# Optimization experiments

Hardware: AMD Instinct MI355X
Metric: run time of the kernel (lower is better)

## Reference

```python
import jax, jax.numpy as jnp
import numpy as np

N_NODES = 50000
N_EDGES = 100000
NUM_GRAPHS = 1024
EMB = 600
NUM_ATOMIC = 119      # Num_atomic_number
NUM_HYB = 8           # HybridizationType values
NUM_AROM = 2
NUM_CHIR = 4          # ChiralType values
NUM_CHARGE = 9
NUM_BOND_TYPE = 22    # BondType values


def setup_inputs() -> dict:
    key = jax.random.key(0)
    ks = jax.random.split(key, 20)
    # integer graph data
    atom = jnp.stack([
        jax.random.randint(ks[0], (N_NODES,), 0, NUM_ATOMIC),
        jax.random.randint(ks[1], (N_NODES,), 0, NUM_HYB),
        jax.random.randint(ks[2], (N_NODES,), 0, NUM_AROM),
        jax.random.randint(ks[3], (N_NODES,), 0, NUM_CHIR),
        jax.random.randint(ks[4], (N_NODES,), 0, NUM_CHARGE),
    ], axis=1)
    bond_index = jax.random.randint(ks[5], (2, N_EDGES), 0, N_NODES)
    bond_attr = jnp.stack([
        jax.random.randint(ks[6], (N_EDGES,), 0, NUM_BOND_TYPE),
        jax.random.randint(ks[7], (N_EDGES,), 0, NUM_ATOMIC),
    ], axis=1)
    batch = jnp.sort(jax.random.randint(ks[8], (N_NODES,), 0, NUM_GRAPHS))
    # parameters (kaiming-uniform-ish scale)
    def emb(k, n, d):
        bound = float(np.sqrt(6.0 / d))
        return jax.random.uniform(k, (n, d), minval=-bound, maxval=bound, dtype=jnp.float32)
    def lin(k, out_d, in_d):
        bound = float(np.sqrt(6.0 / in_d))
        return jax.random.uniform(k, (out_d, in_d), minval=-bound, maxval=bound, dtype=jnp.float32)
    return {
        "atom": atom, "bond_index": bond_index, "bond_attr": bond_attr, "batch": batch,
        "W_atom_num": emb(ks[9], NUM_ATOMIC, EMB),
        "W_hyb": emb(ks[10], NUM_HYB, EMB),
        "W_arom": emb(ks[11], NUM_AROM, EMB),
        "W_chir": emb(ks[12], NUM_CHIR, EMB),
        "W_charge": emb(ks[13], NUM_CHARGE, EMB),
        "W_bond_type": emb(ks[14], NUM_BOND_TYPE, EMB),
        "W_bond_atom_i": emb(ks[15], NUM_ATOMIC, EMB),
        "W_sl_atom": emb(ks[16], NUM_ATOMIC, EMB),
        "W_sl": emb(ks[17], 1, EMB),
        "W1": lin(ks[18], EMB, EMB), "b1": jnp.zeros((EMB,), jnp.float32),
        "W2": lin(ks[19], EMB // 2, EMB), "b2": jnp.zeros((EMB // 2,), jnp.float32),
        "W3": lin(jax.random.fold_in(key, 99), 1, EMB // 2),
    }


def reference(atom, bond_index, bond_attr, batch,
              W_atom_num, W_hyb, W_arom, W_chir, W_charge,
              W_bond_type, W_bond_atom_i, W_sl_atom, W_sl,
              W1, b1, W2, b2, W3):
    N = atom.shape[0]
    # Step 1: node embedding = sum of 5 lookups  [N, EMB]
    node = (W_atom_num[atom[:, 0]] + W_hyb[atom[:, 1]] + W_arom[atom[:, 2]]
            + W_chir[atom[:, 3]] + W_charge[atom[:, 4]])
    # Step 2: edge embeddings; self-loops appended after real bonds
    bond_emb = W_bond_type[bond_attr[:, 0]] + W_bond_atom_i[bond_attr[:, 1]]  # [E, EMB]
    sl_emb = W_sl_atom[atom[:, 0]] + W_sl[0]                                  # [N, EMB]
    edge_emb = jnp.concatenate([bond_emb, sl_emb], axis=0)                    # [E+N, EMB]
    loop = jnp.arange(N, dtype=bond_index.dtype)
    src = jnp.concatenate([bond_index[0], loop])
    dst = jnp.concatenate([bond_index[1], loop])
    # Step 3: 2 message-passing layers: gather src, multiply edge_emb, scatter-add to dst
    for _ in range(2):
        node = jax.ops.segment_sum(node[src] * edge_emb, dst, num_segments=N)
    # Step 4: energy MLP  ReLU -> Linear(d,d) -> ReLU -> Linear(d,d/2) -> ReLU -> Linear(d/2,1)
    h = jax.nn.relu(node)
    h = jax.nn.relu(h @ W1.T + b1)
    h = jax.nn.relu(h @ W2.T + b2)
    node_energy = h @ W3.T  # [N, 1]
    # Step 5: global add pool per graph
    dg = jax.ops.segment_sum(node_energy, batch, num_segments=NUM_GRAPHS)  # [NUM_GRAPHS, 1]
    return dg
```

## Files before the change

### kernel.cpp

```cpp
#include <hip/hip_runtime.h>

#define EMB 600
#define Q4  150
#define KP  608

typedef unsigned short ushortT;
typedef __attribute__((ext_vector_type(8))) short short8;
typedef __attribute__((ext_vector_type(4))) short short4v;
typedef __attribute__((ext_vector_type(4))) float f32x4;

__device__ __forceinline__ float4 f4add(float4 a, float4 b) {
    return make_float4(a.x + b.x, a.y + b.y, a.z + b.z, a.w + b.w);
}
__device__ __forceinline__ float4 f4fma(float4 acc, float4 v, float4 e) {
    return make_float4(fmaf(v.x, e.x, acc.x), fmaf(v.y, e.y, acc.y),
                       fmaf(v.z, e.z, acc.z), fmaf(v.w, e.w, acc.w));
}
__device__ __forceinline__ ushortT bf16_rne(float x) {
    unsigned u = __float_as_uint(x);
    return (ushortT)((u + 0x7fffu + ((u >> 16) & 1u)) >> 16);
}
__device__ __forceinline__ float bf16_to_f(ushortT h) {
    return __uint_as_float(((unsigned)h) << 16);
}

__device__ __forceinline__ size_t frag_off(int row, int col) {
    return ((size_t)((row >> 4) * 19 + (col >> 5)) * 64
            + (row & 15) + 16 * ((col >> 3) & 3)) * 8 + (col & 7);
}

__global__ void k_node_embed(const int* __restrict__ atom,
                             const float4* __restrict__ Wa,
                             const float4* __restrict__ Wh,
                             const float4* __restrict__ War,
                             const float4* __restrict__ Wc,
                             const float4* __restrict__ Wch,
                             float4* __restrict__ out, int N) {
    int idx = blockIdx.x * blockDim.x + threadIdx.x;
    int total = N * Q4;
    if (idx >= total) return;
    int n = idx / Q4;
    int q = idx - n * Q4;
    const int* a = atom + n * 5;
    float4 r = Wa[a[0] * Q4 + q];
    r = f4add(r, Wh [a[1] * Q4 + q]);
    r = f4add(r, War[a[2] * Q4 + q]);
    r = f4add(r, Wc [a[3] * Q4 + q]);
    r = f4add(r, Wch[a[4] * Q4 + q]);
    out[idx] = r;
}

__global__ void k_hist(const int* __restrict__ bdst, int* __restrict__ counts, int E) {
    int i = blockIdx.x * blockDim.x + threadIdx.x;
    if (i < E) atomicAdd(&counts[bdst[i]], 1);
}

__global__ __launch_bounds__(256) void k_scan_l1(const int* __restrict__ counts,
                                                 int* __restrict__ offsets,
                                                 int* __restrict__ blocksums, int N) {
    __shared__ int s[256];
    int t = threadIdx.x;
    int i = blockIdx.x * 256 + t;
    int v = (i < N) ? counts[i] : 0;
    s[t] = v;
    __syncthreads();
#pragma unroll
    for (int off = 1; off < 256; off <<= 1) {
        int x = (t >= off) ? s[t - off] : 0;
        __syncthreads();
        s[t] += x;
        __syncthreads();
    }
    if (i < N) offsets[i] = s[t] - v;
    if (t == 255) blocksums[blockIdx.x] = s[255];
}

__global__ __launch_bounds__(256) void k_scan_l2(int* __restrict__ blocksums,
                                                 int* __restrict__ blockpref, int nb) {
    __shared__ int s[256];
    int t = threadIdx.x;
    int v = (t < nb) ? blocksums[t] : 0;
    s[t] = v;
    __syncthreads();
#pragma unroll
    for (int off = 1; off < 256; off <<= 1) {
        int x = (t >= off) ? s[t - off] : 0;
        __syncthreads();
        s[t] += x;
        __syncthreads();
    }
    if (t < nb) blockpref[t] = s[t] - v;
}

__global__ __launch_bounds__(256) void k_scan_l3(int* __restrict__ offsets,
                                                 int* __restrict__ cursor,
                                                 const int* __restrict__ blockpref, int N) {
    int i = blockIdx.x * 256 + threadIdx.x;
    if (i < N) {
        int o = offsets[i] + blockpref[blockIdx.x];
        offsets[i] = o;
        cursor[i]  = o;
    }
}

__global__ void k_scatter(const int* __restrict__ bdst, int* __restrict__ cursor,
                          int* __restrict__ edge_list, int E) {
    int i = blockIdx.x * blockDim.x + threadIdx.x;
    if (i < E) {
        int pos = atomicAdd(&cursor[bdst[i]], 1);
        edge_list[pos] = i;
    }
}

__global__ __launch_bounds__(256) void k_mp_gather(
        const int* __restrict__ bsrc, const int* __restrict__ battr,
        const int* __restrict__ atom,
        const int* __restrict__ offsets, const int* __restrict__ counts,
        const int* __restrict__ edge_list,
        const float4* __restrict__ Wbt, const float4* __restrict__ Wbai,
        const float4* __restrict__ Wsla, const float4* __restrict__ Wsl,
        const float4* __restrict__ in, float4* __restrict__ out, int N) {
    int wid  = (int)((blockIdx.x * blockDim.x + threadIdx.x) >> 6);
    int lane = threadIdx.x & 63;
    int d    = wid >> 1;
    int half = wid & 1;
    if (d >= N) return;
    int q1 = 75 * half + lane;
    int q2 = q1 + 64;
    bool has2 = lane < 11;

    int start = offsets[d], cnt = counts[d];
    int s = 0, t0 = 0, t1 = 0;
    if (cnt > 0) {
        int eid = edge_list[start];
        s  = bsrc[eid];
        t0 = battr[eid * 2 + 0];
        t1 = battr[eid * 2 + 1];
    }

    const float4* slA = Wsla + atom[d * 5] * Q4;
    const float4* inr = in + (size_t)d * Q4;
    float4 acc1 = make_float4(0, 0, 0, 0), acc2 = acc1;
    acc1 = f4fma(acc1, inr[q1], f4add(slA[q1], Wsl[q1]));
    if (has2) acc2 = f4fma(acc2, inr[q2], f4add(slA[q2], Wsl[q2]));

    for (int k = 0; k < cnt; k++) {
        int ns = s, nt0 = t0, nt1 = t1;
        if (k + 1 < cnt) {
            int ne = edge_list[start + k + 1];
            ns  = bsrc[ne];
            nt0 = battr[ne * 2 + 0];
            nt1 = battr[ne * 2 + 1];
        }
        const float4* e0 = Wbt  + t0 * Q4;
        const float4* e1 = Wbai + t1 * Q4;
        const float4* sr = in + (size_t)s * Q4;
        acc1 = f4fma(acc1, sr[q1], f4add(e0[q1], e1[q1]));
        if (has2) acc2 = f4fma(acc2, sr[q2], f4add(e0[q2], e1[q2]));
        s = ns; t0 = nt0; t1 = nt1;
    }
    float4* orow = out + (size_t)d * Q4;
    orow[q1] = acc1;
    if (has2) orow[q2] = acc2;
}

__device__ __forceinline__ void frag_store4h(ushortT* __restrict__ hi,
                                             int d, int q, float4 v) {
    int kc = q >> 3, ks = (q >> 1) & 3, halfw = q & 1;
    size_t off = ((size_t)((d >> 4) * 19 + kc) * 64 + (d & 15) + 16 * ks) * 8
                 + halfw * 4;
    float vv[4] = {v.x, v.y, v.z, v.w};
    short4v h4;
#pragma unroll
    for (int j = 0; j < 4; j++)
        h4[j] = (short)bf16_rne(fmaxf(vv[j], 0.f));
    *(short4v*)(hi + off) = h4;
}

__global__ __launch_bounds__(256) void k_mp_gather_rs(
        const int* __restrict__ bsrc, const int* __restrict__ battr,
        const int* __restrict__ atom,
        const int* __restrict__ offsets, const int* __restrict__ counts,
        const int* __restrict__ edge_list,
        const float4* __restrict__ Wbt, const float4* __restrict__ Wbai,
        const float4* __restrict__ Wsla, const float4* __restrict__ Wsl,
        const float4* __restrict__ in,
        ushortT* __restrict__ hi, int N) {
    int wid  = (int)((blockIdx.x * blockDim.x + threadIdx.x) >> 6);
    int lane = threadIdx.x & 63;
    int d    = wid >> 1;
    int half = wid & 1;
    if (d >= N) return;
    int q1 = 75 * half + lane;
    int q2 = q1 + 64;
    bool has2 = lane < 11;

    int start = offsets[d], cnt = counts[d];
    int s = 0, t0 = 0, t1 = 0;
    if (cnt > 0) {
        int eid = edge_list[start];
        s  = bsrc[eid];
        t0 = battr[eid * 2 + 0];
        t1 = battr[eid * 2 + 1];
    }

    const float4* slA = Wsla + atom[d * 5] * Q4;
    const float4* inr = in + (size_t)d * Q4;
    float4 acc1 = make_float4(0, 0, 0, 0), acc2 = acc1;
    acc1 = f4fma(acc1, inr[q1], f4add(slA[q1], Wsl[q1]));
    if (has2) acc2 = f4fma(acc2, inr[q2], f4add(slA[q2], Wsl[q2]));

    for (int k = 0; k < cnt; k++) {
        int ns = s, nt0 = t0, nt1 = t1;
        if (k + 1 < cnt) {
            int ne = edge_list[start + k + 1];
            ns  = bsrc[ne];
            nt0 = battr[ne * 2 + 0];
            nt1 = battr[ne * 2 + 1];
        }
        const float4* e0 = Wbt  + t0 * Q4;
        const float4* e1 = Wbai + t1 * Q4;
        const float4* sr = in + (size_t)s * Q4;
        acc1 = f4fma(acc1, sr[q1], f4add(e0[q1], e1[q1]));
        if (has2) acc2 = f4fma(acc2, sr[q2], f4add(e0[q2], e1[q2]));
        s = ns; t0 = nt0; t1 = nt1;
    }
    frag_store4h(hi, d, q1, acc1);
    if (has2) frag_store4h(hi, d, q2, acc2);
    if (half == 0 && lane == 31) {
        size_t off = ((size_t)((d >> 4) * 19 + 18) * 64 + (d & 15) + 48) * 8;
        short8 z = {0, 0, 0, 0, 0, 0, 0, 0};
        *(short8*)(hi + off) = z;
    }
}

__global__ void k_split_w_frag(const float* __restrict__ src,
                               short8* __restrict__ dhi, short8* __restrict__ dlo,
                               int rows_in, int cb_count) {
    int idx = blockIdx.x * blockDim.x + threadIdx.x;
    int total = cb_count * 19 * 64;
    if (idx >= total) return;
    int lane = idx & 63;
    int tile = idx >> 6;
    int cb = tile / 19, kc = tile - cb * 19;
    int col = cb * 16 + (lane & 15);
    int k0  = kc * 32 + (lane >> 4) * 8;
    short8 h, l;
#pragma unroll
    for (int j = 0; j < 8; j++) {
        int k = k0 + j;
        float x = (col < rows_in && k < 600) ? src[(size_t)col * 600 + k] : 0.f;
        ushortT hh = bf16_rne(x);
        h[j] = (short)hh;
        l[j] = (short)bf16_rne(x - bf16_to_f(hh));
    }
    dhi[idx] = h;
    dlo[idx] = l;
}

struct FragSet { short8 a[4], bh[4], bl[4]; };

__device__ __forceinline__ void frag_load(FragSet& f,
        const short8* __restrict__ Af,
        const short8* __restrict__ Bfh, const short8* __restrict__ Bfl,
        int aBase, int bBase, int kc) {
    int ak = aBase + kc * 64;
    int bk = bBase + kc * 64;
#pragma unroll
    for (int i = 0; i < 4; i++) {
        f.a[i]  = Af [ak + i * 1216];
        f.bh[i] = Bfh[bk + i * 1216];
        f.bl[i] = Bfl[bk + i * 1216];
    }
}

__device__ __forceinline__ void frag_mfma(const FragSet& f, f32x4 acc[4][4]) {
#pragma unroll
    for (int i = 0; i < 4; i++)
#pragma unroll
        for (int j = 0; j < 4; j++) {
            acc[i][j] = __builtin_amdgcn_mfma_f32_16x16x32_bf16(f.a[i], f.bh[j], acc[i][j], 0, 0, 0);
            acc[i][j] = __builtin_amdgcn_mfma_f32_16x16x32_bf16(f.a[i], f.bl[j], acc[i][j], 0, 0, 0);
        }
}

__device__ __forceinline__ void gemm_core_reg(
        const short8* __restrict__ Af,
        const short8* __restrict__ Bfh, const short8* __restrict__ Bfl,
        int aBase, int bBase, f32x4 acc[4][4]) {
    for (int kc = 0; kc < 19; kc++) {
        FragSet f;
        frag_load(f, Af, Bfh, Bfl, aBase, bBase, kc);
        frag_mfma(f, acc);
    }
}

__device__ __forceinline__ void decode_wg(int ncb, int& rowblk, int& colblk) {
    int nwg  = gridDim.x;
    int orig = blockIdx.x;
    int q = nwg >> 3, r = nwg & 7;
    int xcd = orig & 7, rank = orig >> 3;
    int wgid = (xcd < r ? xcd * (q + 1) : r * (q + 1) + (xcd - r) * q) + rank;
    rowblk = wgid / ncb;
    colblk = wgid - rowblk * ncb;
}

__global__ __launch_bounds__(256, 4) void k_gemm1r(
        const short8* __restrict__ Af,
        const short8* __restrict__ Wfh, const short8* __restrict__ Wfl,
        const float* __restrict__ b1,
        ushortT* __restrict__ Hf, int N) {
    int rowblk, colblk;
    decode_wg(5, rowblk, colblk);
    int row0 = rowblk * 128;
    int col0 = colblk * 128;
    int t = threadIdx.x, w = t >> 6, l = t & 63;
    int wr = w >> 1, wc = w & 1, fr = l & 15, fq = l >> 4;

    int aBase = (rowblk * 8 + wr * 4) * 1216 + l;
    int bBase = (colblk * 8 + wc * 4) * 1216 + l;
    f32x4 acc[4][4];
#pragma unroll
    for (int i = 0; i < 4; i++)
#pragma unroll
        for (int j = 0; j < 4; j++) acc[i][j] = f32x4{0.f, 0.f, 0.f, 0.f};
    gemm_core_reg(Af, Wfh, Wfl, aBase, bBase, acc);

#pragma unroll
    for (int i = 0; i < 4; i++) {
#pragma unroll
        for (int j = 0; j < 4; j++) {
            int col = col0 + wc * 64 + j * 16 + fr;
            float bias = (col < 600) ? b1[col] : 0.f;
#pragma unroll
            for (int r = 0; r < 4; r++) {
                int row = row0 + wr * 64 + i * 16 + fq * 4 + r;
                if (row >= N) continue;
                if (col < 600) {
                    float x = fmaxf(acc[i][j][r] + bias, 0.f);
                    Hf[frag_off(row, col)] = bf16_rne(x);
                } else if (col < KP) {
                    Hf[frag_off(row, col)] = 0;
                }
            }
        }
    }
}

__global__ __launch_bounds__(256, 4) void k_gemm2r(
        const short8* __restrict__ Af,
        const short8* __restrict__ Wfh, const short8* __restrict__ Wfl,
        const float* __restrict__ b2, const float* __restrict__ W3,
        float* __restrict__ energy, int N) {
    __shared__ float sE[128];
    int rowblk, colblk;
    decode_wg(3, rowblk, colblk);
    int row0 = rowblk * 128;
    int col0 = colblk * 128;
    int t = threadIdx.x, w = t >> 6, l = t & 63;
    int wr = w >> 1, wc = w & 1, fr = l & 15, fq = l >> 4;

    int aBase = (rowblk * 8 + wr * 4) * 1216 + l;
    int bBase = (colblk * 8 + wc * 4) * 1216 + l;
    f32x4 acc[4][4];
#pragma unroll
    for (int i = 0; i < 4; i++)
#pragma unroll
        for (int j = 0; j < 4; j++) acc[i][j] = f32x4{0.f, 0.f, 0.f, 0.f};
    gemm_core_reg(Af, Wfh, Wfl, aBase, bBase, acc);

    if (t < 128) sE[t] = 0.f;
    __syncthreads();
#pragma unroll
    for (int i = 0; i < 4; i++) {
        float p[4] = {0.f, 0.f, 0.f, 0.f};
#pragma unroll
        for (int j = 0; j < 4; j++) {
            int col = col0 + wc * 64 + j * 16 + fr;
            if (col < 300) {
                float bias = b2[col];
                float wv   = W3[col];
#pragma unroll
                for (int r = 0; r < 4; r++)
                    p[r] += fmaxf(acc[i][j][r] + bias, 0.f) * wv;
            }
        }
#pragma unroll
        for (int r = 0; r < 4; r++) {
            float v = p[r];
            v += __shfl_xor(v, 1, 64);
            v += __shfl_xor(v, 2, 64);
            v += __shfl_xor(v, 4, 64);
            v += __shfl_xor(v, 8, 64);
            p[r] = v;
        }
        if (fr == 0) {
#pragma unroll
            for (int r = 0; r < 4; r++)
                atomicAdd(&sE[wr * 64 + i * 16 + fq * 4 + r], p[r]);
        }
    }
    __syncthreads();
    if (t < 128) {
        int row = row0 + t;
        if (row < N) atomicAdd(&energy[row], sE[t]);
    }
}

__global__ void k_pool(const float* __restrict__ energy, const int* __restrict__ batch,
                       float* __restrict__ dg, int N) {
    int i = blockIdx.x * blockDim.x + threadIdx.x;
    int lane = threadIdx.x & 63;
    float v = (i < N) ? energy[i] : 0.f;
    int   b = (i < N) ? batch[i]  : -1;
#pragma unroll
    for (int off = 1; off < 64; off <<= 1) {
        float vv = __shfl_down(v, off, 64);
        int   bb = __shfl_down(b, off, 64);
        if (lane + off < 64 && bb == b) v += vv;
    }
    int pb = __shfl_up(b, 1, 64);
    if (i < N && (lane == 0 || pb != b)) atomicAdd(&dg[b], v);
}

extern "C" void kernel_launch(void* const* d_in, const int* in_sizes, int n_in,
                              void* d_out, int out_size, void* d_ws, size_t ws_size,
                              hipStream_t stream) {
    const int* atom       = (const int*)d_in[0];
    const int* bond_index = (const int*)d_in[1];
    const int* bond_attr  = (const int*)d_in[2];
    const int* batch      = (const int*)d_in[3];
    const float* Wa   = (const float*)d_in[4];
    const float* Wh   = (const float*)d_in[5];
    const float* War  = (const float*)d_in[6];
    const float* Wc   = (const float*)d_in[7];
    const float* Wch  = (const float*)d_in[8];
    const float* Wbt  = (const float*)d_in[9];
    const float* Wbai = (const float*)d_in[10];
    const float* Wsla = (const float*)d_in[11];
    const float* Wsl  = (const float*)d_in[12];
    const float* W1   = (const float*)d_in[13];
    const float* b1   = (const float*)d_in[14];
    const float* W2   = (const float*)d_in[15];
    const float* b2   = (const float*)d_in[16];
    const float* W3   = (const float*)d_in[17];

    int N = in_sizes[0] / 5;
    int E = in_sizes[1] / 2;
    int Mb = (N + 127) / 128;
    int Npad = Mb * 128;
    int nTiles = Npad / 16;
    int nb = (N + 255) / 256;

    size_t regionBytes = (size_t)Npad * KP * 4;
    char* base = (char*)d_ws;
    float* nodeA = (float*)base;
    float* nodeB = (float*)(base + regionBytes);
    short8* Af = (short8*)nodeA;
    short8* Hf = (short8*)nodeB;
    char* tail = base + 2 * regionBytes;
    float* energy  = (float*)tail;
    int* counts    = (int*)(energy + N);
    int* offsets   = counts + N;
    int* cursor    = offsets + N;
    int* edge_list = cursor + N;
    short8* W1fh   = (short8*)(edge_list + E);
    short8* W1fl   = W1fh + 40 * 19 * 64;
    short8* W2fh   = W1fl + 40 * 19 * 64;
    short8* W2fl   = W2fh + 24 * 19 * 64;
    int* blocksums = (int*)(W2fl + 24 * 19 * 64);
    int* blockpref = blocksums + 256;

    const int* bsrc = bond_index;
    const int* bdst = bond_index + E;

    hipMemsetAsync(counts, 0, (size_t)N * sizeof(int), stream);
    k_hist<<<(E + 255) / 256, 256, 0, stream>>>(bdst, counts, E);
    k_scan_l1<<<nb, 256, 0, stream>>>(counts, offsets, blocksums, N);
    k_scan_l2<<<1, 256, 0, stream>>>(blocksums, blockpref, nb);
    k_scan_l3<<<nb, 256, 0, stream>>>(offsets, cursor, blockpref, N);
    k_scatter<<<(E + 255) / 256, 256, 0, stream>>>(bdst, cursor, edge_list, E);

    k_split_w_frag<<<(40 * 19 * 64 + 255) / 256, 256, 0, stream>>>(W1, W1fh, W1fl, 600, 40);
    k_split_w_frag<<<(24 * 19 * 64 + 255) / 256, 256, 0, stream>>>(W2, W2fh, W2fl, 300, 24);

    {
        int total = N * Q4;
        k_node_embed<<<(total + 255) / 256, 256, 0, stream>>>(
            atom, (const float4*)Wa, (const float4*)Wh, (const float4*)War,
            (const float4*)Wc, (const float4*)Wch, (float4*)nodeA, N);
    }

    int mpblocks = (2 * N * 64 + 255) / 256;
    k_mp_gather<<<mpblocks, 256, 0, stream>>>(bsrc, bond_attr, atom,
        offsets, counts, edge_list,
        (const float4*)Wbt, (const float4*)Wbai, (const float4*)Wsla, (const float4*)Wsl,
        (const float4*)nodeA, (float4*)nodeB, N);

    {
        int firstPad = N / 16;
        size_t offB  = (size_t)firstPad * 1216 * 16;
        size_t cntB  = (size_t)(nTiles - firstPad) * 1216 * 16;
        if (cntB) hipMemsetAsync((char*)Af + offB, 0, cntB, stream);
    }

    k_mp_gather_rs<<<mpblocks, 256, 0, stream>>>(bsrc, bond_attr, atom,
        offsets, counts, edge_list,
        (const float4*)Wbt, (const float4*)Wbai, (const float4*)Wsla, (const float4*)Wsl,
        (const float4*)nodeB, (ushortT*)Af, N);

    k_gemm1r<<<Mb * 5, 256, 0, stream>>>(Af, W1fh, W1fl, b1, (ushortT*)Hf, N);

    hipMemsetAsync(energy, 0, (size_t)N * sizeof(float), stream);
    k_gemm2r<<<Mb * 3, 256, 0, stream>>>(Hf, W2fh, W2fl, b2, W3, energy, N);

    hipMemsetAsync(d_out, 0, (size_t)out_size * sizeof(float), stream);
    k_pool<<<(N + 255) / 256, 256, 0, stream>>>(energy, batch, (float*)d_out, N);
}
```

Before: 392.4 us.

## Store layer-1 node features in bf16 and drop lo-split weight MFMAs

The first message-passing layer now writes its output as bf16 instead of fp32, and the second layer gathers bf16 rows and converts them to float, halving the intermediate traffic. The MLP GEMMs drop the hi/lo bf16 split of the weights and use a single bf16 weight copy, halving the MFMA count and the weight-fragment loads. In exchange, precision falls in both the intermediate node features and the weights, which may affect tolerance against the fp32 reference.

After: 348.9 us. -11.1%, faster.

```diff
diff --git a/kernel.cpp b/kernel.cpp
--- a/kernel.cpp
+++ b/kernel.cpp
@@ -22,6 +22,18 @@
 }
 __device__ __forceinline__ float bf16_to_f(ushortT h) {
     return __uint_as_float(((unsigned)h) << 16);
+}
+__device__ __forceinline__ short4v f4_to_bf4(float4 v) {
+    short4v r;
+    r[0] = (short)bf16_rne(v.x);
+    r[1] = (short)bf16_rne(v.y);
+    r[2] = (short)bf16_rne(v.z);
+    r[3] = (short)bf16_rne(v.w);
+    return r;
+}
+__device__ __forceinline__ float4 bf4_to_f4(short4v h) {
+    return make_float4(bf16_to_f((ushortT)h[0]), bf16_to_f((ushortT)h[1]),
+                       bf16_to_f((ushortT)h[2]), bf16_to_f((ushortT)h[3]));
 }
 
 __device__ __forceinline__ size_t frag_off(int row, int col) {
@@ -112,14 +124,14 @@
     }
 }
 
-__global__ __launch_bounds__(256) void k_mp_gather(
+__global__ __launch_bounds__(256) void k_mp_gather_b(
         const int* __restrict__ bsrc, const int* __restrict__ battr,
         const int* __restrict__ atom,
         const int* __restrict__ offsets, const int* __restrict__ counts,
         const int* __restrict__ edge_list,
         const float4* __restrict__ Wbt, const float4* __restrict__ Wbai,
         const float4* __restrict__ Wsla, const float4* __restrict__ Wsl,
-        const float4* __restrict__ in, float4* __restrict__ out, int N) {
+        const float4* __restrict__ in, ushortT* __restrict__ out, int N) {
     int wid  = (int)((blockIdx.x * blockDim.x + threadIdx.x) >> 6);
     int lane = threadIdx.x & 63;
     int d    = wid >> 1;
@@ -159,9 +171,9 @@
         if (has2) acc2 = f4fma(acc2, sr[q2], f4add(e0[q2], e1[q2]));
         s = ns; t0 = nt0; t1 = nt1;
     }
-    float4* orow = out + (size_t)d * Q4;
-    orow[q1] = acc1;
-    if (has2) orow[q2] = acc2;
+    ushortT* orow = out + (size_t)d * EMB;
+    *(short4v*)(orow + q1 * 4) = f4_to_bf4(acc1);
+    if (has2) *(short4v*)(orow + q2 * 4) = f4_to_bf4(acc2);
 }
 
 __device__ __forceinline__ void frag_store4h(ushortT* __restrict__ hi,
@@ -184,7 +196,7 @@
         const int* __restrict__ edge_list,
         const float4* __restrict__ Wbt, const float4* __restrict__ Wbai,
         const float4* __restrict__ Wsla, const float4* __restrict__ Wsl,
-        const float4* __restrict__ in,
+        const ushortT* __restrict__ in,
         ushortT* __restrict__ hi, int N) {
     int wid  = (int)((blockIdx.x * blockDim.x + threadIdx.x) >> 6);
     int lane = threadIdx.x & 63;
@@ -205,10 +217,12 @@
     }
 
     const float4* slA = Wsla + atom[d * 5] * Q4;
-    const float4* inr = in + (size_t)d * Q4;
+    const ushortT* inr = in + (size_t)d * EMB;
     float4 acc1 = make_float4(0, 0, 0, 0), acc2 = acc1;
-    acc1 = f4fma(acc1, inr[q1], f4add(slA[q1], Wsl[q1]));
-    if (has2) acc2 = f4fma(acc2, inr[q2], f4add(slA[q2], Wsl[q2]));
+    acc1 = f4fma(acc1, bf4_to_f4(*(const short4v*)(inr + q1 * 4)),
+                 f4add(slA[q1], Wsl[q1]));
+    if (has2) acc2 = f4fma(acc2, bf4_to_f4(*(const short4v*)(inr + q2 * 4)),
+                           f4add(slA[q2], Wsl[q2]));
 
     for (int k = 0; k < cnt; k++) {
         int ns = s, nt0 = t0, nt1 = t1;
@@ -220,9 +234,11 @@
         }
         const float4* e0 = Wbt  + t0 * Q4;
         const float4* e1 = Wbai + t1 * Q4;
-        const float4* sr = in + (size_t)s * Q4;
-        acc1 = f4fma(acc1, sr[q1], f4add(e0[q1], e1[q1]));
-        if (has2) acc2 = f4fma(acc2, sr[q2], f4add(e0[q2], e1[q2]));
+        const ushortT* sr = in + (size_t)s * EMB;
+        acc1 = f4fma(acc1, bf4_to_f4(*(const short4v*)(sr + q1 * 4)),
+                     f4add(e0[q1], e1[q1]));
+        if (has2) acc2 = f4fma(acc2, bf4_to_f4(*(const short4v*)(sr + q2 * 4)),
+                               f4add(e0[q2], e1[q2]));
         s = ns; t0 = nt0; t1 = nt1;
     }
     frag_store4h(hi, d, q1, acc1);
@@ -235,7 +251,7 @@
 }
 
 __global__ void k_split_w_frag(const float* __restrict__ src,
-                               short8* __restrict__ dhi, short8* __restrict__ dlo,
+                               short8* __restrict__ dst,
                                int rows_in, int cb_count) {
     int idx = blockIdx.x * blockDim.x + threadIdx.x;
     int total = cb_count * 19 * 64;
@@ -245,32 +261,27 @@
     int cb = tile / 19, kc = tile - cb * 19;
     int col = cb * 16 + (lane & 15);
     int k0  = kc * 32 + (lane >> 4) * 8;
-    short8 h, l;
+    short8 h;
 #pragma unroll
     for (int j = 0; j < 8; j++) {
         int k = k0 + j;
         float x = (col < rows_in && k < 600) ? src[(size_t)col * 600 + k] : 0.f;
-        ushortT hh = bf16_rne(x);
-        h[j] = (short)hh;
-        l[j] = (short)bf16_rne(x - bf16_to_f(hh));
-    }
-    dhi[idx] = h;
-    dlo[idx] = l;
-}
-
-struct FragSet { short8 a[4], bh[4], bl[4]; };
+        h[j] = (short)bf16_rne(x);
+    }
+    dst[idx] = h;
+}
+
+struct FragSet { short8 a[4], b[4]; };
 
 __device__ __forceinline__ void frag_load(FragSet& f,
-        const short8* __restrict__ Af,
-        const short8* __restrict__ Bfh, const short8* __restrict__ Bfl,
+        const short8* __restrict__ Af, const short8* __restrict__ Bf,
         int aBase, int bBase, int kc) {
     int ak = aBase + kc * 64;
     int bk = bBase + kc * 64;
 #pragma unroll
     for (int i = 0; i < 4; i++) {
-        f.a[i]  = Af [ak + i * 1216];
-        f.bh[i] = Bfh[bk + i * 1216];
-        f.bl[i] = Bfl[bk + i * 1216];
+        f.a[i] = Af[ak + i * 1216];
+        f.b[i] = Bf[bk + i * 1216];
     }
 }
 
@@ -278,19 +289,16 @@
 #pragma unroll
     for (int i = 0; i < 4; i++)
 #pragma unroll
-        for (int j = 0; j < 4; j++) {
-            acc[i][j] = __builtin_amdgcn_mfma_f32_16x16x32_bf16(f.a[i], f.bh[j], acc[i][j], 0, 0, 0);
-            acc[i][j] = __builtin_amdgcn_mfma_f32_16x16x32_bf16(f.a[i], f.bl[j], acc[i][j], 0, 0, 0);
-        }
+        for (int j = 0; j < 4; j++)
+            acc[i][j] = __builtin_amdgcn_mfma_f32_16x16x32_bf16(f.a[i], f.b[j], acc[i][j], 0, 0, 0);
 }
 
 __device__ __forceinline__ void gemm_core_reg(
-        const short8* __restrict__ Af,
-        const short8* __restrict__ Bfh, const short8* __restrict__ Bfl,
+        const short8* __restrict__ Af, const short8* __restrict__ Bf,
         int aBase, int bBase, f32x4 acc[4][4]) {
     for (int kc = 0; kc < 19; kc++) {
         FragSet f;
-        frag_load(f, Af, Bfh, Bfl, aBase, bBase, kc);
+        frag_load(f, Af, Bf, aBase, bBase, kc);
         frag_mfma(f, acc);
     }
 }
@@ -306,8 +314,7 @@
 }
 
 __global__ __launch_bounds__(256, 4) void k_gemm1r(
-        const short8* __restrict__ Af,
-        const short8* __restrict__ Wfh, const short8* __restrict__ Wfl,
+        const short8* __restrict__ Af, const short8* __restrict__ Wf,
         const float* __restrict__ b1,
         ushortT* __restrict__ Hf, int N) {
     int rowblk, colblk;
@@ -324,7 +331,7 @@
     for (int i = 0; i < 4; i++)
 #pragma unroll
         for (int j = 0; j < 4; j++) acc[i][j] = f32x4{0.f, 0.f, 0.f, 0.f};
-    gemm_core_reg(Af, Wfh, Wfl, aBase, bBase, acc);
+    gemm_core_reg(Af, Wf, aBase, bBase, acc);
 
 #pragma unroll
     for (int i = 0; i < 4; i++) {
@@ -348,8 +355,7 @@
 }
 
 __global__ __launch_bounds__(256, 4) void k_gemm2r(
-        const short8* __restrict__ Af,
-        const short8* __restrict__ Wfh, const short8* __restrict__ Wfl,
+        const short8* __restrict__ Af, const short8* __restrict__ Wf,
         const float* __restrict__ b2, const float* __restrict__ W3,
         float* __restrict__ energy, int N) {
     __shared__ float sE[128];
@@ -367,7 +373,7 @@
     for (int i = 0; i < 4; i++)
 #pragma unroll
         for (int j = 0; j < 4; j++) acc[i][j] = f32x4{0.f, 0.f, 0.f, 0.f};
-    gemm_core_reg(Af, Wfh, Wfl, aBase, bBase, acc);
+    gemm_core_reg(Af, Wf, aBase, bBase, acc);
 
     if (t < 128) sE[t] = 0.f;
     __syncthreads();
@@ -455,20 +461,18 @@
     size_t regionBytes = (size_t)Npad * KP * 4;
     char* base = (char*)d_ws;
     float* nodeA = (float*)base;
-    float* nodeB = (float*)(base + regionBytes);
+    ushortT* nodeBh = (ushortT*)(base + regionBytes);
     short8* Af = (short8*)nodeA;
-    short8* Hf = (short8*)nodeB;
+    short8* Hf = (short8*)nodeBh;
     char* tail = base + 2 * regionBytes;
     float* energy  = (float*)tail;
     int* counts    = (int*)(energy + N);
     int* offsets   = counts + N;
     int* cursor    = offsets + N;
     int* edge_list = cursor + N;
-    short8* W1fh   = (short8*)(edge_list + E);
-    short8* W1fl   = W1fh + 40 * 19 * 64;
-    short8* W2fh   = W1fl + 40 * 19 * 64;
-    short8* W2fl   = W2fh + 24 * 19 * 64;
-    int* blocksums = (int*)(W2fl + 24 * 19 * 64);
+    short8* W1f    = (short8*)(edge_list + E);
+    short8* W2f    = W1f + 40 * 19 * 64;
+    int* blocksums = (int*)(W2f + 24 * 19 * 64);
     int* blockpref = blocksums + 256;
 
     const int* bsrc = bond_index;
@@ -481,8 +485,8 @@
     k_scan_l3<<<nb, 256, 0, stream>>>(offsets, cursor, blockpref, N);
     k_scatter<<<(E + 255) / 256, 256, 0, stream>>>(bdst, cursor, edge_list, E);
 
-    k_split_w_frag<<<(40 * 19 * 64 + 255) / 256, 256, 0, stream>>>(W1, W1fh, W1fl, 600, 40);
-    k_split_w_frag<<<(24 * 19 * 64 + 255) / 256, 256, 0, stream>>>(W2, W2fh, W2fl, 300, 24);
+    k_split_w_frag<<<(40 * 19 * 64 + 255) / 256, 256, 0, stream>>>(W1, W1f, 600, 40);
+    k_split_w_frag<<<(24 * 19 * 64 + 255) / 256, 256, 0, stream>>>(W2, W2f, 300, 24);
 
     {
         int total = N * Q4;
@@ -492,10 +496,10 @@
     }
 
     int mpblocks = (2 * N * 64 + 255) / 256;
-    k_mp_gather<<<mpblocks, 256, 0, stream>>>(bsrc, bond_attr, atom,
+    k_mp_gather_b<<<mpblocks, 256, 0, stream>>>(bsrc, bond_attr, atom,
         offsets, counts, edge_list,
         (const float4*)Wbt, (const float4*)Wbai, (const float4*)Wsla, (const float4*)Wsl,
-        (const float4*)nodeA, (float4*)nodeB, N);
+        (const float4*)nodeA, nodeBh, N);
 
     {
         int firstPad = N / 16;
@@ -507,12 +511,12 @@
     k_mp_gather_rs<<<mpblocks, 256, 0, stream>>>(bsrc, bond_attr, atom,
         offsets, counts, edge_list,
         (const float4*)Wbt, (const float4*)Wbai, (const float4*)Wsla, (const float4*)Wsl,
-        (const float4*)nodeB, (ushortT*)Af, N);
-
-    k_gemm1r<<<Mb * 5, 256, 0, stream>>>(Af, W1fh, W1fl, b1, (ushortT*)Hf, N);
+        nodeBh, (ushortT*)Af, N);
+
+    k_gemm1r<<<Mb * 5, 256, 0, stream>>>(Af, W1f, b1, (ushortT*)Hf, N);
 
     hipMemsetAsync(energy, 0, (size_t)N * sizeof(float), stream);
-    k_gemm2r<<<Mb * 3, 256, 0, stream>>>(Hf, W2fh, W2fl, b2, W3, energy, N);
+    k_gemm2r<<<Mb * 3, 256, 0, stream>>>(Hf, W2f, b2, W3, energy, N);
 
     hipMemsetAsync(d_out, 0, (size_t)out_size * sizeof(float), stream);
     k_pool<<<(N + 255) / 256, 256, 0, stream>>>(energy, batch, (float*)d_out, N);
```
